# Optimization experiments

Hardware: AMD Instinct MI355X
Metric: run time of the kernel (lower is better)

Reference implementation:

```python
import jax, jax.numpy as jnp
import numpy as np

# Fixed Gauss-Legendre quadrature on [-A, A] replacing scipy.integrate.quadrature
A = 5.0
NQ = 64
_x, _w = np.polynomial.legendre.leggauss(NQ)
GL_X = jnp.asarray(_x * A, dtype=jnp.float32)  # nodes scaled to [-5, 5]
# Fold exp(-z^2/2)/sqrt(2*pi) and interval scaling into the weights
GL_W_EFF = jnp.asarray(_w * A * np.exp(-(_x * A) ** 2 / 2.0) / np.sqrt(2.0 * np.pi), dtype=jnp.float32)

# given_params=True constants
SIG_M1, SIG_M2, SIG_I = 1.0, 1.0, 1.0
SIG_M1N1, SIG_M2N2 = 1.0, 0.5
SIG_N1I, SIG_N2I = 0.5, 1.9
SIG_M1W, SIG_M2W = 2.8, -2.2
TAU, DT = 100.0, 20.0


def setup_inputs() -> dict:
    key = jax.random.key(0)
    B, T = 8192, 2048
    u = jax.random.normal(key, (B, T), dtype=jnp.float32)
    return {"u": u}


def reference(u):
    B, T = u.shape
    alpha = jnp.float32(DT / TAU)

    def step(carry, u_t):
        k1, k2, v = carry  # each [B]
        delta = jnp.sqrt(SIG_M1**2 * k1**2 + SIG_M2**2 * k2**2 + SIG_I**2 * u_t**2)  # [B]
        # gauss_int[b] = int_{-A}^{A} (1 - tanh(delta_b z)^2) exp(-z^2/2) dz / sqrt(2pi)
        dphi = 1.0 - jnp.tanh(delta[:, None] * GL_X[None, :]) ** 2  # [B, NQ]
        gauss_int = dphi @ GL_W_EFF  # [B]
        k1_new = k1 + (-k1 + SIG_M1N1 * gauss_int * k1 + SIG_N1I * gauss_int * v) * alpha
        k2_new = k2 + (-k2 + SIG_M2N2 * gauss_int * k2 + SIG_N2I * gauss_int * v) * alpha
        v_new = v + (-v + u_t) * alpha
        z = SIG_M1W * k1_new + SIG_M2W * k2_new
        return (k1_new, k2_new, v_new), z

    zeros = jnp.zeros((B,), dtype=u.dtype)
    _, z_seq = jax.lax.scan(step, (zeros, zeros, zeros), u.T)  # z_seq: [T, B]
    # z_hist: [B, T+1], column 0 is the zero initial state
    z_hist = jnp.concatenate([zeros[:, None], z_seq.T], axis=1)
    return z_hist
```

## Files before the change

kernel.cpp:

```cpp
#include <hip/hip_runtime.h>
#include <math.h>


#define Bsz   8192
#define Tlen  2048
#define TP1   2049
#define NQ    64
#define NG    2049
#define NTAB2 2048
#define INV_H 32.0f
#define CHUNKS 16
#define CLEN  128
#define WARM  128
#define BLOCK 256
#define SIM_GRID (32 * CHUNKS)
#define SROW  33

#define WS_TAB 128

__device__ __forceinline__ void bar_nodrain() {
    asm volatile("s_waitcnt lgkmcnt(0)" ::: "memory");
    __builtin_amdgcn_s_barrier();
}
__device__ __forceinline__ void ds_fence() {
    asm volatile("s_waitcnt lgkmcnt(0)" ::: "memory");
}

__global__ __launch_bounds__(256) void setup_kernel(float* __restrict__ ws,
                                                    float* __restrict__ out) {
    __shared__ float  fx[NQ], fw[NQ];
    __shared__ double inv[NQ + 1];
    const int tid = threadIdx.x;
    if (tid <= NQ) inv[tid] = (tid == 0) ? 0.0 : 1.0 / (double)tid;
    __syncthreads();
    if (tid < NQ) {
        double z = cos(3.14159265358979323846 * (tid + 0.75) / (NQ + 0.5));
        double p1 = 1.0, p2 = 0.0, pp = 1.0;
        for (int it = 0; it < 4; ++it) {
            p1 = 1.0; p2 = 0.0;
            for (int j = 1; j <= NQ; ++j) {
                double p3 = p2; p2 = p1;
                p1 = ((2.0 * j - 1.0) * z * p2 - (j - 1.0) * p3) * inv[j];
            }
            pp = NQ * (z * p1 - p2) / (z * z - 1.0);
            if (it < 3) z -= p1 / pp;
        }
        double w  = 2.0 / ((1.0 - z * z) * pp * pp);
        double xs = z * 5.0;
        fx[tid] = (float)xs;
        fw[tid] = (float)(w * 5.0 * exp(-0.5 * xs * xs) * 0.3989422804014327);
    }
    __syncthreads();
    const int j = blockIdx.x * 256 + tid;
    if (j < NG) {
        const float d = sqrtf((float)j * (1.0f / INV_H));
        float acc = 0.0f;
        #pragma unroll 8
        for (int q = 0; q < NQ; ++q) {
            float t = tanhf(d * fx[q]);
            acc = fmaf(fw[q], 1.0f - t * t, acc);
        }
        ws[WS_TAB + j] = acc;
    }
    out[(size_t)j * TP1] = 0.0f;
}

__device__ __forceinline__ float step_one(float uu, float& k1, float& k2,
                                          float& v, const float2* s_tab) {
    float s   = fmaf(k1, k1, fmaf(k2, k2, uu * uu));
    float idx = fminf(s * INV_H, 2046.999f);
    int   i0  = (int)idx;
    float f   = idx - (float)i0;
    float2 g2 = s_tab[i0];
    float g   = fmaf(f, g2.y - g2.x, g2.x);
    float gv  = g * v;
    float nk1 = fmaf(k1, fmaf(0.2f, g, 0.8f), 0.10f * gv);
    float nk2 = fmaf(k2, fmaf(0.1f, g, 0.8f), 0.38f * gv);
    v  = fmaf(0.2f, uu - v, v);
    k1 = nk1; k2 = nk2;
    return fmaf(2.8f, nk1, -2.2f * nk2);
}

#define GLOAD(G, t) { _Pragma("unroll")                                       \
    for (int r = 0; r < 8; ++r)                                               \
        G[r] = *(const float4*)(up + (size_t)r * 8 * Tlen + (t)); }

#define STAGE(G) { asm volatile("" ::: "memory");  _Pragma("unroll")          \
    for (int r = 0; r < 8; ++r) {                                             \
        int b8 = (8 * r + srow) * SROW + scol;                                \
        sb[b8] = G[r].x; sb[b8+1] = G[r].y; sb[b8+2] = G[r].z;                \
        sb[b8+3] = G[r].w; }                                                  \
    ds_fence(); }

__global__ __launch_bounds__(BLOCK, 2) void sim_kernel(const float* __restrict__ u,
                                                       const float* __restrict__ ws,
                                                       float* __restrict__ out) {
    __shared__ float2 s_tab[NTAB2];
    __shared__ float  s_st[4][64 * SROW];
    const int tid = threadIdx.x;
    const int w   = tid >> 6;
    const int l   = tid & 63;
    float* sb = s_st[w];

    const int c    = blockIdx.x >> 5;
    const int bb   = blockIdx.x & 31;
    const int rowb = bb * 256 + w * 64;
    const int t_out   = c * CLEN;
    const int t_begin = (t_out >= WARM) ? (t_out - WARM) : 0;

    const int srow = l >> 3;
    const int scol = (l & 7) * 4;
    const float* __restrict__ up = u + (size_t)(rowb + srow) * Tlen + scol;
    const int lbase = l * SROW;

    float4 G0[8], G1[8];
    GLOAD(G0, t_begin);
    GLOAD(G1, t_begin + 32);

    {
        const float* g = ws + WS_TAB;
        #pragma unroll
        for (int i = 0; i < NTAB2 / (BLOCK * 4); ++i) {
            int k = (i * BLOCK + tid) * 4;
            float4 a = *(const float4*)(g + k);
            float  b = g[k + 4];
            s_tab[k + 0] = make_float2(a.x, a.y);
            s_tab[k + 1] = make_float2(a.y, a.z);
            s_tab[k + 2] = make_float2(a.z, a.w);
            s_tab[k + 3] = make_float2(a.w, b);
        }
    }
    bar_nodrain();

    float k1 = 0.f, k2 = 0.f, v = 0.f;

    for (int tb = t_begin; tb + 64 <= t_out; tb += 64) {
        STAGE(G0);
        GLOAD(G0, tb + 64);
        #pragma unroll
        for (int t2 = 0; t2 < 32; ++t2)
            step_one(sb[lbase + t2], k1, k2, v, s_tab);
        STAGE(G1);
        GLOAD(G1, tb + 96);
        #pragma unroll
        for (int t2 = 0; t2 < 32; ++t2)
            step_one(sb[lbase + t2], k1, k2, v, s_tab);
    }

    const int col = l & 31;
    const int rh  = l >> 5;
    for (int h = 0; h < 2; ++h) {
        float zz[64];
        const int tb = t_out + h * 64;
        {
            STAGE(G0);
            int tn = tb + 64; if (tn > Tlen - 32) tn = Tlen - 32;
            GLOAD(G0, tn);
            #pragma unroll
            for (int t2 = 0; t2 < 32; ++t2)
                zz[t2] = step_one(sb[lbase + t2], k1, k2, v, s_tab);
        }
        {
            STAGE(G1);
            int tn = tb + 96; if (tn > Tlen - 32) tn = Tlen - 32;
            GLOAD(G1, tn);
            #pragma unroll
            for (int t2 = 0; t2 < 32; ++t2)
                zz[32 + t2] = step_one(sb[lbase + t2], k1, k2, v, s_tab);
        }
        const int cb = t_out + 1 + h * 64;
        #pragma unroll
        for (int p = 0; p < 2; ++p) {
            asm volatile("" ::: "memory");
            #pragma unroll
            for (int j = 0; j < 32; ++j)
                sb[lbase + j] = zz[p * 32 + j];
            ds_fence();
            #pragma unroll
            for (int k = 0; k < 32; ++k) {
                int row = 2 * k + rh;
                out[(size_t)(rowb + row) * TP1 + cb + p * 32 + col] =
                    sb[row * SROW + col];
            }
            ds_fence();
        }
    }
}

extern "C" void kernel_launch(void* const* d_in, const int* in_sizes, int n_in,
                              void* d_out, int out_size, void* d_ws, size_t ws_size,
                              hipStream_t stream) {
    const float* u = (const float*)d_in[0];
    float* out = (float*)d_out;
    float* ws  = (float*)d_ws;
    setup_kernel<<<32, 256, 0, stream>>>(ws, out);
    sim_kernel<<<SIM_GRID, BLOCK, 0, stream>>>(u, ws, out);
}
```

Before: 145.0 us.

## Read staged inputs into registers and use a single load buffer pipeline

The two register buffers of global loads (G0/G1) become one, and each 32-step slice of inputs is copied from LDS into a register array before the next slice is staged and its global load is issued. The recurrence then reads from registers instead of LDS, and the output flushes sit between compute blocks. This lowers register pressure from the duplicate load buffers and takes LDS reads off the serial dependency chain. The cost is an extra LDS readback and a shorter prefetch distance, which may leave less global-load latency hidden.

```diff
diff --git a/kernel.cpp b/kernel.cpp
--- a/kernel.cpp
+++ b/kernel.cpp
@@ -92,6 +92,23 @@
         sb[b8+3] = G[r].w; }                                                  \
     ds_fence(); }
 
+#define READBACK() { asm volatile("" ::: "memory"); _Pragma("unroll")         \
+    for (int j = 0; j < 32; ++j) U[j] = sb[lbase + j];                        \
+    ds_fence(); }
+
+#define FLUSH(h) { const int cb = t_out + 1 + 64 * (h);                       \
+    _Pragma("unroll") for (int p = 0; p < 2; ++p) {                           \
+        asm volatile("" ::: "memory");                                        \
+        _Pragma("unroll") for (int j = 0; j < 32; ++j)                        \
+            sb[lbase + j] = zz[p * 32 + j];                                   \
+        ds_fence();                                                           \
+        _Pragma("unroll") for (int kk = 0; kk < 32; ++kk) {                   \
+            int row = 2 * kk + rh;                                            \
+            out[(size_t)(rowb + row) * TP1 + cb + p * 32 + col] =             \
+                sb[row * SROW + col];                                         \
+        }                                                                     \
+        ds_fence(); } }
+
 __global__ __launch_bounds__(BLOCK, 2) void sim_kernel(const float* __restrict__ u,
                                                        const float* __restrict__ ws,
                                                        float* __restrict__ out) {
@@ -113,9 +130,8 @@
     const float* __restrict__ up = u + (size_t)(rowb + srow) * Tlen + scol;
     const int lbase = l * SROW;
 
-    float4 G0[8], G1[8];
-    GLOAD(G0, t_begin);
-    GLOAD(G1, t_begin + 32);
+    float4 G[8];
+    GLOAD(G, t_begin);
 
     {
         const float* g = ws + WS_TAB;
@@ -132,59 +148,38 @@
     }
     bar_nodrain();
 
+    STAGE(G);
+    GLOAD(G, t_begin + 32);
+
     float k1 = 0.f, k2 = 0.f, v = 0.f;
+    float U[32];
 
-    for (int tb = t_begin; tb + 64 <= t_out; tb += 64) {
-        STAGE(G0);
-        GLOAD(G0, tb + 64);
+    for (int tb = t_begin; tb < t_out; tb += 32) {
+        READBACK();
+        STAGE(G);
+        GLOAD(G, tb + 64);
         #pragma unroll
         for (int t2 = 0; t2 < 32; ++t2)
-            step_one(sb[lbase + t2], k1, k2, v, s_tab);
-        STAGE(G1);
-        GLOAD(G1, tb + 96);
-        #pragma unroll
-        for (int t2 = 0; t2 < 32; ++t2)
-            step_one(sb[lbase + t2], k1, k2, v, s_tab);
+            step_one(U[t2], k1, k2, v, s_tab);
     }
 
     const int col = l & 31;
     const int rh  = l >> 5;
-    for (int h = 0; h < 2; ++h) {
-        float zz[64];
-        const int tb = t_out + h * 64;
-        {
-            STAGE(G0);
-            int tn = tb + 64; if (tn > Tlen - 32) tn = Tlen - 32;
-            GLOAD(G0, tn);
-            #pragma unroll
-            for (int t2 = 0; t2 < 32; ++t2)
-                zz[t2] = step_one(sb[lbase + t2], k1, k2, v, s_tab);
-        }
-        {
-            STAGE(G1);
-            int tn = tb + 96; if (tn > Tlen - 32) tn = Tlen - 32;
-            GLOAD(G1, tn);
-            #pragma unroll
-            for (int t2 = 0; t2 < 32; ++t2)
-                zz[32 + t2] = step_one(sb[lbase + t2], k1, k2, v, s_tab);
-        }
-        const int cb = t_out + 1 + h * 64;
+    float zz[64];
+    #pragma unroll
+    for (int k = 0; k < 4; ++k) {
+        const int tb = t_out + 32 * k;
+        READBACK();
+        if (k == 2) FLUSH(0);
+        STAGE(G);
+        int tn = tb + 64;
+        if (tn > Tlen - 32) tn = Tlen - 32;
+        GLOAD(G, tn);
         #pragma unroll
-        for (int p = 0; p < 2; ++p) {
-            asm volatile("" ::: "memory");
-            #pragma unroll
-            for (int j = 0; j < 32; ++j)
-                sb[lbase + j] = zz[p * 32 + j];
-            ds_fence();
-            #pragma unroll
-            for (int k = 0; k < 32; ++k) {
-                int row = 2 * k + rh;
-                out[(size_t)(rowb + row) * TP1 + cb + p * 32 + col] =
-                    sb[row * SROW + col];
-            }
-            ds_fence();
-        }
+        for (int t2 = 0; t2 < 32; ++t2)
+            zz[(k & 1) * 32 + t2] = step_one(U[t2], k1, k2, v, s_tab);
     }
+    FLUSH(1);
 }
 
 extern "C" void kernel_launch(void* const* d_in, const int* in_sizes, int n_in,
```

Result: no change. 145.3 us (+0.2%).
